# Kernel tuning notes

Hardware: AMD Instinct MI355X
Metric: run time of the kernel (lower is better)

Reference implementation:

```python
import jax, jax.numpy as jnp
import numpy as np

H, W = 256, 256
S, S_IDX, END_BIAS = 48, 3, 10
E_IDX = S - END_BIAS          # 38
N_ITER = E_IDX - (S_IDX + 1)  # 34 sequential segments after the start segment
OUT_WIN = 10                  # outlier1d window length
OUT_THRESH = 2.0


def setup_inputs() -> dict:
    key = jax.random.key(0)
    # (x, y) event coordinates in [0, W) x [0, H); t/p/b columns are unused by the module.
    events = jax.random.uniform(key, (16, 960000, 2), jnp.float32, minval=0.0, maxval=256.0)
    return {"events": events}


def _blur(a):
    """5x5 uniform (0.04) blur, SAME padding; a: [B, S, D] -> [B, S, D]."""
    k = jnp.full((1, 1, 5, 5), 0.04, jnp.float32)
    return jax.lax.conv_general_dilated(a[:, None], k, (1, 1), [(2, 2), (2, 2)])[:, 0]


def _outlier_flags(m):
    """outlier1d(m[b, si:si+10], thresh=2)[0] for si in [S_IDX+1, E_IDX). m: [B,S] -> bool [B,N_ITER]."""
    widx = (jnp.arange(N_ITER)[:, None] + S_IDX + 1) + jnp.arange(OUT_WIN)[None, :]
    w = m[:, widx]                                   # [B, N_ITER, 10]
    med = jnp.median(w, axis=-1, keepdims=True)
    diff = jnp.abs(w - med)
    mad = jnp.median(diff, axis=-1)                  # [B, N_ITER]
    return 0.6745 * diff[..., 0] / mad > OUT_THRESH


def reference(events):
    B, N, _ = events.shape
    segmentLen = N // S            # static python int
    Nu = segmentLen * S
    x = events[:, :Nu, 0].astype(jnp.int32)   # [B, Nu]
    y = events[:, :Nu, 1].astype(jnp.int32)
    chunks = jnp.repeat(jnp.arange(S), segmentLen)   # segment id per event, [Nu]
    bidx = jnp.arange(B)[:, None]

    # per-batch x-t / y-t histograms via scatter-add
    alongX = jnp.zeros((B, S, W), jnp.float32).at[bidx, chunks[None, :], x].add(1.0)
    alongY = jnp.zeros((B, S, H), jnp.float32).at[bidx, chunks[None, :], y].add(1.0)

    def proc_axis(along, D):
        flat = along.reshape(B, -1)
        cv = (flat.mean(-1) + 3.0 * jnp.std(flat, axis=-1, ddof=1))[:, None, None]
        a = _blur(jnp.clip(along, 0.0, cv))
        m = jnp.einsum('bsd,d->bs', a, jnp.arange(D, dtype=jnp.float32)) / segmentLen
        start = m[:, S_IDX:S_IDX + 1]
        aligned = jnp.round(m - start - (D // 2 - start)).astype(jnp.int32)
        return m, aligned

    meanX, alignedX = proc_axis(alongX, W)
    meanY, alignedY = proc_axis(alongY, H)
    is_out = _outlier_flags(meanX) | _outlier_flags(meanY)   # [B, N_ITER]

    def per_batch(xb, yb, aX, aY, outb):
        xs = jnp.clip(xb - aX[chunks], 0, W - 1)
        ys = jnp.clip(yb - aY[chunks], 0, H - 1)
        idx_c = (xs + W * ys).reshape(S, segmentLen)
        idx_v = (xs // 2 + (W // 2) * (ys // 2)).reshape(S, segmentLen)
        container0 = jnp.zeros(W * H, jnp.int32).at[idx_c[S_IDX]].add(1)
        ver0 = jnp.zeros((W // 2) * (H // 2), bool).at[idx_v[S_IDX]].set(True)

        def step(carry, inp):
            container, ver, stopped = carry
            ic, iv, is_o = inp
            ver_new = ver.at[iv].set(True)
            cnt = jnp.sum(ver_new).astype(jnp.float32)
            new_info = jnp.sum(jnp.logical_xor(ver_new, ver)).astype(jnp.float32)
            brk = new_info / cnt < 0.1
            do = (~stopped) & (~is_o) & (~brk)
            stopped = stopped | ((~stopped) & (~is_o) & brk)
            container = jnp.where(do, container.at[ic].add(1), container)
            ver = jnp.where(do, ver_new, ver)
            return (container, ver, stopped), None

        (container, _, _), _ = jax.lax.scan(
            step, (container0, ver0, jnp.array(False)),
            (idx_c[S_IDX + 1:E_IDX], idx_v[S_IDX + 1:E_IDX], outb))
        c = container.astype(jnp.float32)
        cv = c.mean() + 3.0 * jnp.std(c, ddof=1)
        return jnp.clip(c, 0.0, cv) / cv

    containers = jax.vmap(per_batch)(x, y, alignedX, alignedY, is_out)  # [B, W*H]
    return containers.reshape(B, 1, H, W)
```

## Files before the change

kernel.cpp:

```cpp
#include <hip/hip_runtime.h>

#define NB 16
#define NEV 960000
#define NS 48
#define SEG 20000
#define S_IDX 3
#define E_IDX 38
#define N_ITER 34
#define ND 256
#define NCH 35

__global__ __launch_bounds__(256) void hist_kernel(const float* __restrict__ events,
                                                   float* __restrict__ alongX,
                                                   float* __restrict__ alongY,
                                                   unsigned* __restrict__ compact,
                                                   unsigned* __restrict__ container,
                                                   unsigned* __restrict__ masks,
                                                   unsigned long long* __restrict__ sums,
                                                   unsigned long long* __restrict__ cvsums) {
    __shared__ unsigned hx[4][ND], hy[4][ND];
    __shared__ unsigned long long qredX[4], qredY[4];
    int tid = threadIdx.x;
    int blk = blockIdx.x;
    int b = blk / NS, c = blk % NS;
    int wave = tid >> 6, lane = tid & 63;
    #pragma unroll
    for (int j = 0; j < 4; j++) { hx[j][tid] = 0; hy[j][tid] = 0; }
    {
        uint4 z = {0u, 0u, 0u, 0u};
        for (int i = blk * 256 + tid; i < 262144; i += NB * NS * 256)
            ((uint4*)container)[i] = z;
        for (int i = blk * 256 + tid; i < 71680; i += NB * NS * 256)
            ((uint4*)masks)[i] = z;
        if (blk == 0 && tid < NB * 2) sums[tid] = 0ull;
        if (blk == 1 && tid < NB * 2) cvsums[tid] = 0ull;
    }
    __syncthreads();
    size_t base = (size_t)b * NEV + (size_t)c * SEG;
    const float4* ev4 = (const float4*)(events + base * 2);
    bool wr = (c >= S_IDX && c < E_IDX);
    uint4* dst = wr ? (uint4*)(compact + ((size_t)b * NCH + (c - S_IDX)) * (SEG / 2)) : nullptr;
    unsigned* HX = hx[wave];
    unsigned* HY = hy[wave];
    for (int k = tid; k < SEG / 8; k += 256) {
        float4 v0 = ev4[4 * k], v1 = ev4[4 * k + 1], v2 = ev4[4 * k + 2], v3 = ev4[4 * k + 3];
        int x0 = (int)v0.x, y0 = (int)v0.y, x1 = (int)v0.z, y1 = (int)v0.w;
        int x2 = (int)v1.x, y2 = (int)v1.y, x3 = (int)v1.z, y3 = (int)v1.w;
        int x4 = (int)v2.x, y4 = (int)v2.y, x5 = (int)v2.z, y5 = (int)v2.w;
        int x6 = (int)v3.x, y6 = (int)v3.y, x7 = (int)v3.z, y7 = (int)v3.w;
        x0 = x0 > 255 ? 255 : x0; y0 = y0 > 255 ? 255 : y0;
        x1 = x1 > 255 ? 255 : x1; y1 = y1 > 255 ? 255 : y1;
        x2 = x2 > 255 ? 255 : x2; y2 = y2 > 255 ? 255 : y2;
        x3 = x3 > 255 ? 255 : x3; y3 = y3 > 255 ? 255 : y3;
        x4 = x4 > 255 ? 255 : x4; y4 = y4 > 255 ? 255 : y4;
        x5 = x5 > 255 ? 255 : x5; y5 = y5 > 255 ? 255 : y5;
        x6 = x6 > 255 ? 255 : x6; y6 = y6 > 255 ? 255 : y6;
        x7 = x7 > 255 ? 255 : x7; y7 = y7 > 255 ? 255 : y7;
        atomicAdd(&HX[x0], 1u); atomicAdd(&HY[y0], 1u);
        atomicAdd(&HX[x1], 1u); atomicAdd(&HY[y1], 1u);
        atomicAdd(&HX[x2], 1u); atomicAdd(&HY[y2], 1u);
        atomicAdd(&HX[x3], 1u); atomicAdd(&HY[y3], 1u);
        atomicAdd(&HX[x4], 1u); atomicAdd(&HY[y4], 1u);
        atomicAdd(&HX[x5], 1u); atomicAdd(&HY[y5], 1u);
        atomicAdd(&HX[x6], 1u); atomicAdd(&HY[y6], 1u);
        atomicAdd(&HX[x7], 1u); atomicAdd(&HY[y7], 1u);
        if (wr) {
            uint4 p;
            p.x = (unsigned)(x0 | (y0 << 8)) | ((unsigned)(x1 | (y1 << 8)) << 16);
            p.y = (unsigned)(x2 | (y2 << 8)) | ((unsigned)(x3 | (y3 << 8)) << 16);
            p.z = (unsigned)(x4 | (y4 << 8)) | ((unsigned)(x5 | (y5 << 8)) << 16);
            p.w = (unsigned)(x6 | (y6 << 8)) | ((unsigned)(x7 | (y7 << 8)) << 16);
            dst[k] = p;
        }
    }
    __syncthreads();
    unsigned sx = hx[0][tid] + hx[1][tid] + hx[2][tid] + hx[3][tid];
    unsigned sy = hy[0][tid] + hy[1][tid] + hy[2][tid] + hy[3][tid];
    int o = (b * NS + c) * ND + tid;
    alongX[o] = (float)sx;
    alongY[o] = (float)sy;
    unsigned long long qx = (unsigned long long)sx * sx;
    unsigned long long qy = (unsigned long long)sy * sy;
    for (int off = 32; off; off >>= 1) { qx += __shfl_down(qx, off); qy += __shfl_down(qy, off); }
    if (lane == 0) { qredX[wave] = qx; qredY[wave] = qy; }
    __syncthreads();
    if (tid == 0) {
        atomicAdd(&cvsums[b * 2],     qredX[0] + qredX[1] + qredX[2] + qredX[3]);
        atomicAdd(&cvsums[b * 2 + 1], qredY[0] + qredY[1] + qredY[2] + qredY[3]);
    }
}

__global__ __launch_bounds__(256) void stats_kernel(const float* __restrict__ alongX,
                                                    const float* __restrict__ alongY,
                                                    const unsigned long long* __restrict__ cvsums,
                                                    int* __restrict__ alignedX,
                                                    int* __restrict__ alignedY,
                                                    float* __restrict__ m_all) {
    __shared__ float sbuf[16 * ND];
    int tid = threadIdx.x;
    int blk = blockIdx.x;
    int g = blk & 3, axis = (blk >> 2) & 1, b = blk >> 3;
    const float* along = (axis ? alongY : alongX) + (size_t)b * NS * ND;
    int rbase = g * 12 - 2;
    for (int j = 0; j < 16; j++) {
        int r = rbase + j;
        if (r >= 0 && r < NS) sbuf[j * ND + tid] = along[r * ND + tid];
    }
    double ts  = 960000.0;
    double ts2 = (double)cvsums[b * 2 + axis];
    const double N = (double)(NS * ND);
    double mean = ts / N;
    double var  = (ts2 - ts * ts / N) / (N - 1.0);
    float cv = (float)(mean + 3.0 * sqrt(var));
    __syncthreads();
    int wave = tid >> 6, lane = tid & 63;
    for (int q = 0; q < 3; ++q) {
        int sI = g * 12 + wave * 3 + q;
        double acc = 0.0;
        #pragma unroll
        for (int k = 0; k < 4; ++k) {
            int d = lane + 64 * k;
            int lo = d - 2 < 0 ? 0 : d - 2;
            int hi = d + 2 > 255 ? 255 : d + 2;
            double Wd = 0.5 * (double)(lo + hi) * (double)(hi - lo + 1);
            double t = 0.0;
            #pragma unroll
            for (int ds = -2; ds <= 2; ++ds) {
                int ss = sI + ds;
                if (ss >= 0 && ss < NS) t += (double)fminf(sbuf[(ss - rbase) * ND + d], cv);
            }
            acc += t * Wd;
        }
        for (int off = 32; off; off >>= 1) acc += __shfl_down(acc, off);
        if (lane == 0) {
            float mf = (float)(acc * 0.04 / (double)SEG);
            m_all[(b * 2 + axis) * NS + sI] = mf;
            (axis ? alignedY : alignedX)[b * NS + sI] = (int)rintf(mf - 128.0f);
        }
    }
}

__global__ __launch_bounds__(256) void mask_kernel(const unsigned* __restrict__ compact,
                                                   const int* __restrict__ alignedX,
                                                   const int* __restrict__ alignedY,
                                                   unsigned* __restrict__ masks) {
    __shared__ unsigned sm[512];
    int tid = threadIdx.x, blk = blockIdx.x;
    int hi = blk & 1;
    int tile = blk >> 1;
    int b = tile / NCH, ci = tile % NCH, si = S_IDX + ci;
    sm[tid] = 0; sm[tid + 256] = 0;
    __syncthreads();
    int aX = alignedX[b * NS + si], aY = alignedY[b * NS + si];
    const uint4* cp = (const uint4*)(compact + ((size_t)b * NCH + ci) * (SEG / 2));
    for (int i = hi * 1250 + tid; i < (hi + 1) * 1250; i += 256) {
        uint4 w = cp[i];
        unsigned wsv[4] = {w.x, w.y, w.z, w.w};
        #pragma unroll
        for (int j = 0; j < 4; j++) {
            unsigned v = wsv[j];
            #pragma unroll
            for (int h = 0; h < 2; h++) {
                unsigned e = (h ? (v >> 16) : v) & 0xFFFFu;
                int xs = (int)(e & 255u) - aX; xs = xs < 0 ? 0 : (xs > 255 ? 255 : xs);
                int ys = (int)(e >> 8)   - aY; ys = ys < 0 ? 0 : (ys > 255 ? 255 : ys);
                int iv = (xs >> 1) | ((ys >> 1) << 7);
                atomicOr(&sm[iv >> 5], 1u << (iv & 31));
            }
        }
    }
    __syncthreads();
    unsigned* mo = masks + (size_t)tile * 512;
    unsigned v0 = sm[tid], v1 = sm[tid + 256];
    if (v0) atomicOr(&mo[tid], v0);
    if (v1) atomicOr(&mo[tid + 256], v1);
}

__device__ inline float median10(const float* v) {
    float w[10];
    #pragma unroll
    for (int i = 0; i < 10; i++) w[i] = v[i];
    #pragma unroll
    for (int i = 1; i < 10; i++) {
        float k = w[i]; int j = i - 1;
        while (j >= 0 && w[j] > k) { w[j + 1] = w[j]; j--; }
        w[j + 1] = k;
    }
    return 0.5f * (w[4] + w[5]);
}

__device__ inline bool outlier_flag(const float* w) {
    float med = median10(w);
    float d[10];
    #pragma unroll
    for (int i = 0; i < 10; i++) d[i] = fabsf(w[i] - med);
    float d0 = d[0];
    float mad = median10(d);
    return (0.6745f * d0 / mad) > 2.0f;
}

__device__ inline unsigned wave_sum_u32(unsigned v) {
    for (int off = 32; off; off >>= 1) v += __shfl_xor(v, off);
    return v;
}

__global__ __launch_bounds__(64) void decide_kernel(const unsigned* __restrict__ masks,
                                                    const float* __restrict__ m_all,
                                                    unsigned long long* __restrict__ commitmask) {
    int b = blockIdx.x, lane = threadIdx.x;
    const unsigned* mb = masks + (size_t)b * NCH * 512;
    uint4 v0 = ((const uint4*)mb)[lane * 2];
    uint4 v1 = ((const uint4*)mb)[lane * 2 + 1];
    const uint4* pp = (const uint4*)(mb + 512);
    uint4 p0 = pp[lane * 2], p1 = pp[lane * 2 + 1];
    bool f = false;
    if (lane < N_ITER) {
        const float* mx = m_all + b * 2 * NS;
        const float* my = mx + NS;
        f = outlier_flag(&mx[S_IDX + 1 + lane]) || outlier_flag(&my[S_IDX + 1 + lane]);
    }
    unsigned long long omask = __ballot(f);
    unsigned ver[8] = {v0.x, v0.y, v0.z, v0.w, v1.x, v1.y, v1.z, v1.w};
    unsigned pc = 0;
    #pragma unroll
    for (int j = 0; j < 8; j++) pc += __popc(ver[j]);
    unsigned cnt = wave_sum_u32(pc);
    unsigned long long cm = 1ull;
    for (int idx = 1; idx < NCH; ++idx) {
        uint4 c0 = p0, c1 = p1;
        if (idx + 1 < NCH) {
            const uint4* np = (const uint4*)(mb + (size_t)(idx + 1) * 512);
            p0 = np[lane * 2]; p1 = np[lane * 2 + 1];
        }
        unsigned del[8] = {c0.x, c0.y, c0.z, c0.w, c1.x, c1.y, c1.z, c1.w};
        unsigned nl = 0;
        #pragma unroll
        for (int j = 0; j < 8; j++) nl += __popc(del[j] & ~ver[j]);
        unsigned ni = wave_sum_u32(nl);
        bool is_o = (omask >> (idx - 1)) & 1;
        if (!is_o) {
            unsigned cn = cnt + ni;
            float ratio = (float)ni / (float)cn;
            if (ratio < 0.1f) break;
            cm |= 1ull << idx;
            cnt = cn;
            #pragma unroll
            for (int j = 0; j < 8; j++) ver[j] |= del[j];
        }
    }
    if (lane == 0) commitmask[b] = cm;
}

__global__ __launch_bounds__(256) void commit_kernel(const unsigned* __restrict__ compact,
                                                     const int* __restrict__ alignedX,
                                                     const int* __restrict__ alignedY,
                                                     const unsigned long long* __restrict__ commitmask,
                                                     unsigned* __restrict__ container) {
    int blk = blockIdx.x, tid = threadIdx.x;
    int qi = blk & 3;
    int tile = blk >> 2;
    int b = tile / NCH, ci = tile % NCH;
    if (!((commitmask[b] >> ci) & 1ull)) return;
    int si = S_IDX + ci;
    int aX = alignedX[b * NS + si], aY = alignedY[b * NS + si];
    unsigned* cont = container + (size_t)b * 65536;
    const uint4* cp = (const uint4*)(compact + ((size_t)b * NCH + ci) * (SEG / 2));
    for (int i = qi * 625 + tid; i < (qi + 1) * 625; i += 256) {
        uint4 w = cp[i];
        unsigned wsv[4] = {w.x, w.y, w.z, w.w};
        #pragma unroll
        for (int j = 0; j < 4; j++) {
            unsigned v = wsv[j];
            #pragma unroll
            for (int h = 0; h < 2; h++) {
                unsigned e = (h ? (v >> 16) : v) & 0xFFFFu;
                int xs = (int)(e & 255u) - aX; xs = xs < 0 ? 0 : (xs > 255 ? 255 : xs);
                int ys = (int)(e >> 8)   - aY; ys = ys < 0 ? 0 : (ys > 255 ? 255 : ys);
                atomicAdd(&cont[xs | (ys << 8)], 1u);
            }
        }
    }
}

__global__ __launch_bounds__(256) void cv_kernel(const unsigned* __restrict__ container,
                                                 unsigned long long* __restrict__ sums) {
    __shared__ unsigned long long sredA[4], sredB[4];
    int tid = threadIdx.x, blk = blockIdx.x;
    int b = blk >> 4, part = blk & 15;
    const uint4* c4 = (const uint4*)(container + (size_t)b * 65536) + part * 1024;
    unsigned long long s = 0, s2 = 0;
    for (int i = tid; i < 1024; i += 256) {
        uint4 v = c4[i];
        s  += (unsigned long long)v.x + v.y + v.z + v.w;
        s2 += (unsigned long long)v.x * v.x + (unsigned long long)v.y * v.y
            + (unsigned long long)v.z * v.z + (unsigned long long)v.w * v.w;
    }
    for (int off = 32; off; off >>= 1) { s += __shfl_down(s, off); s2 += __shfl_down(s2, off); }
    if ((tid & 63) == 0) { sredA[tid >> 6] = s; sredB[tid >> 6] = s2; }
    __syncthreads();
    if (tid == 0) {
        atomicAdd(&sums[b * 2],     sredA[0] + sredA[1] + sredA[2] + sredA[3]);
        atomicAdd(&sums[b * 2 + 1], sredB[0] + sredB[1] + sredB[2] + sredB[3]);
    }
}

__global__ __launch_bounds__(256) void finish_kernel(const unsigned* __restrict__ container,
                                                     const unsigned long long* __restrict__ sums,
                                                     float* __restrict__ out) {
    int g = blockIdx.x * 256 + threadIdx.x;
    int b = g >> 14;
    double ts  = (double)sums[b * 2];
    double ts2 = (double)sums[b * 2 + 1];
    double mean = ts / 65536.0;
    double var  = (ts2 - ts * ts / 65536.0) / 65535.0;
    float cv = (float)(mean + 3.0 * sqrt(var));
    uint4 v = ((const uint4*)container)[g];
    float4 o;
    o.x = fminf((float)v.x, cv) / cv;
    o.y = fminf((float)v.y, cv) / cv;
    o.z = fminf((float)v.z, cv) / cv;
    o.w = fminf((float)v.w, cv) / cv;
    ((float4*)out)[g] = o;
}

extern "C" void kernel_launch(void* const* d_in, const int* in_sizes, int n_in,
                              void* d_out, int out_size, void* d_ws, size_t ws_size,
                              hipStream_t stream) {
    const float* events = (const float*)d_in[0];
    float* out = (float*)d_out;
    char* ws = (char*)d_ws;

    float*    alongX    = (float*)(ws);
    float*    alongY    = (float*)(ws + 786432);
    unsigned* container = (unsigned*)(ws + 1572864);
    int*      alignedX  = (int*)(ws + 5767168);
    int*      alignedY  = (int*)(ws + 5770240);
    float*    m_all     = (float*)(ws + 5773312);
    unsigned long long* commitmask = (unsigned long long*)(ws + 5779456);
    unsigned long long* sums       = (unsigned long long*)(ws + 5779584);
    unsigned long long* cvsums     = (unsigned long long*)(ws + 5779840);
    unsigned* compact   = (unsigned*)(ws + 6291456);
    unsigned* masks     = (unsigned*)(ws + 29360128);

    hist_kernel<<<NB * NS, 256, 0, stream>>>(events, alongX, alongY, compact,
                                             container, masks, sums, cvsums);
    stats_kernel<<<NB * 2 * 4, 256, 0, stream>>>(alongX, alongY, cvsums,
                                                 alignedX, alignedY, m_all);
    mask_kernel<<<NB * NCH * 2, 256, 0, stream>>>(compact, alignedX, alignedY, masks);
    decide_kernel<<<NB, 64, 0, stream>>>(masks, m_all, commitmask);
    commit_kernel<<<NB * NCH * 4, 256, 0, stream>>>(compact, alignedX, alignedY,
                                                    commitmask, container);
    cv_kernel<<<NB * 16, 256, 0, stream>>>(container, sums);
    finish_kernel<<<1024, 256, 0, stream>>>(container, sums, out);
}
```

Before: 269.4 us.

## Fold stats into mask/decide kernels and merge cv with finish

Drops the separate stats kernel. The mask kernel now recomputes the two centroids it needs directly from the histograms, and the decide kernel recomputes all centroids per batch, writing the aligned offsets and keeping m in LDS. The cv reduction and the normalize pass are merged into a single per-batch kernel of 1024 threads, which removes the atomics and the sums buffer. This cuts the pipeline from seven launches to five, at the cost of redundant centroid work and only 16 blocks for both the decide and final kernels.

```diff
diff --git a/kernel.cpp b/kernel.cpp
--- a/kernel.cpp
+++ b/kernel.cpp
@@ -10,13 +10,46 @@
 #define ND 256
 #define NCH 35
 
+__device__ inline void centroid(const float* __restrict__ along,
+                                float cv, int sI, int lane,
+                                float* mf_out, int* ai_out) {
+    double acc = 0.0;
+    #pragma unroll
+    for (int k = 0; k < 4; ++k) {
+        int d = lane + 64 * k;
+        int lo = d - 2 < 0 ? 0 : d - 2;
+        int hi = d + 2 > 255 ? 255 : d + 2;
+        double Wd = 0.5 * (double)(lo + hi) * (double)(hi - lo + 1);
+        double t = 0.0;
+        #pragma unroll
+        for (int ds = -2; ds <= 2; ++ds) {
+            int ss = sI + ds;
+            if (ss >= 0 && ss < NS) t += (double)fminf(along[ss * ND + d], cv);
+        }
+        acc += t * Wd;
+    }
+    for (int off = 32; off; off >>= 1) acc += __shfl_down(acc, off);
+    float mf = (float)(acc * 0.04 / (double)SEG);
+    *mf_out = mf;
+    *ai_out = (int)rintf(mf - 128.0f);
+}
+
+__device__ inline float cv_from_sums(const unsigned long long* __restrict__ cvsums,
+                                     int b, int axis) {
+    double ts  = 960000.0;
+    double ts2 = (double)cvsums[b * 2 + axis];
+    const double N = (double)(NS * ND);
+    double mean = ts / N;
+    double var  = (ts2 - ts * ts / N) / (N - 1.0);
+    return (float)(mean + 3.0 * sqrt(var));
+}
+
 __global__ __launch_bounds__(256) void hist_kernel(const float* __restrict__ events,
                                                    float* __restrict__ alongX,
                                                    float* __restrict__ alongY,
                                                    unsigned* __restrict__ compact,
                                                    unsigned* __restrict__ container,
                                                    unsigned* __restrict__ masks,
-                                                   unsigned long long* __restrict__ sums,
                                                    unsigned long long* __restrict__ cvsums) {
     __shared__ unsigned hx[4][ND], hy[4][ND];
     __shared__ unsigned long long qredX[4], qredY[4];
@@ -32,8 +65,7 @@
             ((uint4*)container)[i] = z;
         for (int i = blk * 256 + tid; i < 71680; i += NB * NS * 256)
             ((uint4*)masks)[i] = z;
-        if (blk == 0 && tid < NB * 2) sums[tid] = 0ull;
-        if (blk == 1 && tid < NB * 2) cvsums[tid] = 0ull;
+        if (blk == 0 && tid < NB * 2) cvsums[tid] = 0ull;
     }
     __syncthreads();
     size_t base = (size_t)b * NEV + (size_t)c * SEG;
@@ -90,68 +122,28 @@
     }
 }
 
-__global__ __launch_bounds__(256) void stats_kernel(const float* __restrict__ alongX,
-                                                    const float* __restrict__ alongY,
-                                                    const unsigned long long* __restrict__ cvsums,
-                                                    int* __restrict__ alignedX,
-                                                    int* __restrict__ alignedY,
-                                                    float* __restrict__ m_all) {
-    __shared__ float sbuf[16 * ND];
-    int tid = threadIdx.x;
-    int blk = blockIdx.x;
-    int g = blk & 3, axis = (blk >> 2) & 1, b = blk >> 3;
-    const float* along = (axis ? alongY : alongX) + (size_t)b * NS * ND;
-    int rbase = g * 12 - 2;
-    for (int j = 0; j < 16; j++) {
-        int r = rbase + j;
-        if (r >= 0 && r < NS) sbuf[j * ND + tid] = along[r * ND + tid];
-    }
-    double ts  = 960000.0;
-    double ts2 = (double)cvsums[b * 2 + axis];
-    const double N = (double)(NS * ND);
-    double mean = ts / N;
-    double var  = (ts2 - ts * ts / N) / (N - 1.0);
-    float cv = (float)(mean + 3.0 * sqrt(var));
-    __syncthreads();
-    int wave = tid >> 6, lane = tid & 63;
-    for (int q = 0; q < 3; ++q) {
-        int sI = g * 12 + wave * 3 + q;
-        double acc = 0.0;
-        #pragma unroll
-        for (int k = 0; k < 4; ++k) {
-            int d = lane + 64 * k;
-            int lo = d - 2 < 0 ? 0 : d - 2;
-            int hi = d + 2 > 255 ? 255 : d + 2;
-            double Wd = 0.5 * (double)(lo + hi) * (double)(hi - lo + 1);
-            double t = 0.0;
-            #pragma unroll
-            for (int ds = -2; ds <= 2; ++ds) {
-                int ss = sI + ds;
-                if (ss >= 0 && ss < NS) t += (double)fminf(sbuf[(ss - rbase) * ND + d], cv);
-            }
-            acc += t * Wd;
-        }
-        for (int off = 32; off; off >>= 1) acc += __shfl_down(acc, off);
-        if (lane == 0) {
-            float mf = (float)(acc * 0.04 / (double)SEG);
-            m_all[(b * 2 + axis) * NS + sI] = mf;
-            (axis ? alignedY : alignedX)[b * NS + sI] = (int)rintf(mf - 128.0f);
-        }
-    }
-}
-
 __global__ __launch_bounds__(256) void mask_kernel(const unsigned* __restrict__ compact,
-                                                   const int* __restrict__ alignedX,
-                                                   const int* __restrict__ alignedY,
+                                                   const float* __restrict__ alongX,
+                                                   const float* __restrict__ alongY,
+                                                   const unsigned long long* __restrict__ cvsums,
                                                    unsigned* __restrict__ masks) {
     __shared__ unsigned sm[512];
+    __shared__ int sal[2];
     int tid = threadIdx.x, blk = blockIdx.x;
     int hi = blk & 1;
     int tile = blk >> 1;
     int b = tile / NCH, ci = tile % NCH, si = S_IDX + ci;
+    int wave = tid >> 6, lane = tid & 63;
     sm[tid] = 0; sm[tid + 256] = 0;
-    __syncthreads();
-    int aX = alignedX[b * NS + si], aY = alignedY[b * NS + si];
+    if (wave < 2) {
+        const float* along = (wave ? alongY : alongX) + (size_t)b * NS * ND;
+        float cv = cv_from_sums(cvsums, b, wave);
+        float mf; int ai;
+        centroid(along, cv, si, lane, &mf, &ai);
+        if (lane == 0) sal[wave] = ai;
+    }
+    __syncthreads();
+    int aX = sal[0], aY = sal[1];
     const uint4* cp = (const uint4*)(compact + ((size_t)b * NCH + ci) * (SEG / 2));
     for (int i = hi * 1250 + tid; i < (hi + 1) * 1250; i += 256) {
         uint4 w = cp[i];
@@ -204,51 +196,74 @@
     return v;
 }
 
-__global__ __launch_bounds__(64) void decide_kernel(const unsigned* __restrict__ masks,
-                                                    const float* __restrict__ m_all,
-                                                    unsigned long long* __restrict__ commitmask) {
-    int b = blockIdx.x, lane = threadIdx.x;
-    const unsigned* mb = masks + (size_t)b * NCH * 512;
-    uint4 v0 = ((const uint4*)mb)[lane * 2];
-    uint4 v1 = ((const uint4*)mb)[lane * 2 + 1];
-    const uint4* pp = (const uint4*)(mb + 512);
-    uint4 p0 = pp[lane * 2], p1 = pp[lane * 2 + 1];
-    bool f = false;
-    if (lane < N_ITER) {
-        const float* mx = m_all + b * 2 * NS;
-        const float* my = mx + NS;
-        f = outlier_flag(&mx[S_IDX + 1 + lane]) || outlier_flag(&my[S_IDX + 1 + lane]);
-    }
-    unsigned long long omask = __ballot(f);
-    unsigned ver[8] = {v0.x, v0.y, v0.z, v0.w, v1.x, v1.y, v1.z, v1.w};
-    unsigned pc = 0;
-    #pragma unroll
-    for (int j = 0; j < 8; j++) pc += __popc(ver[j]);
-    unsigned cnt = wave_sum_u32(pc);
-    unsigned long long cm = 1ull;
-    for (int idx = 1; idx < NCH; ++idx) {
-        uint4 c0 = p0, c1 = p1;
-        if (idx + 1 < NCH) {
-            const uint4* np = (const uint4*)(mb + (size_t)(idx + 1) * 512);
-            p0 = np[lane * 2]; p1 = np[lane * 2 + 1];
-        }
-        unsigned del[8] = {c0.x, c0.y, c0.z, c0.w, c1.x, c1.y, c1.z, c1.w};
-        unsigned nl = 0;
-        #pragma unroll
-        for (int j = 0; j < 8; j++) nl += __popc(del[j] & ~ver[j]);
-        unsigned ni = wave_sum_u32(nl);
-        bool is_o = (omask >> (idx - 1)) & 1;
-        if (!is_o) {
-            unsigned cn = cnt + ni;
-            float ratio = (float)ni / (float)cn;
-            if (ratio < 0.1f) break;
-            cm |= 1ull << idx;
-            cnt = cn;
+__global__ __launch_bounds__(256) void decide_kernel(const unsigned* __restrict__ masks,
+                                                     const float* __restrict__ alongX,
+                                                     const float* __restrict__ alongY,
+                                                     const unsigned long long* __restrict__ cvsums,
+                                                     int* __restrict__ alignedX,
+                                                     int* __restrict__ alignedY,
+                                                     unsigned long long* __restrict__ commitmask) {
+    __shared__ float mlds[2 * NS];
+    int b = blockIdx.x, tid = threadIdx.x;
+    int wave = tid >> 6, lane = tid & 63;
+    float cv0 = cv_from_sums(cvsums, b, 0);
+    float cv1 = cv_from_sums(cvsums, b, 1);
+    for (int q = 0; q < 24; ++q) {
+        int p = wave + 4 * q;
+        int ax = p >= NS;
+        int sI = p - NS * ax;
+        const float* along = (ax ? alongY : alongX) + (size_t)b * NS * ND;
+        float mf; int ai;
+        centroid(along, ax ? cv1 : cv0, sI, lane, &mf, &ai);
+        if (lane == 0) {
+            mlds[ax * NS + sI] = mf;
+            (ax ? alignedY : alignedX)[b * NS + sI] = ai;
+        }
+    }
+    __syncthreads();
+    if (tid < 64) {
+        const unsigned* mb = masks + (size_t)b * NCH * 512;
+        uint4 v0 = ((const uint4*)mb)[lane * 2];
+        uint4 v1 = ((const uint4*)mb)[lane * 2 + 1];
+        const uint4* pp = (const uint4*)(mb + 512);
+        uint4 p0 = pp[lane * 2], p1 = pp[lane * 2 + 1];
+        bool f = false;
+        if (lane < N_ITER) {
+            const float* mx = &mlds[0];
+            const float* my = &mlds[NS];
+            f = outlier_flag(&mx[S_IDX + 1 + lane]) || outlier_flag(&my[S_IDX + 1 + lane]);
+        }
+        unsigned long long omask = __ballot(f);
+        unsigned ver[8] = {v0.x, v0.y, v0.z, v0.w, v1.x, v1.y, v1.z, v1.w};
+        unsigned pc = 0;
+        #pragma unroll
+        for (int j = 0; j < 8; j++) pc += __popc(ver[j]);
+        unsigned cnt = wave_sum_u32(pc);
+        unsigned long long cm = 1ull;
+        for (int idx = 1; idx < NCH; ++idx) {
+            uint4 c0 = p0, c1 = p1;
+            if (idx + 1 < NCH) {
+                const uint4* np = (const uint4*)(mb + (size_t)(idx + 1) * 512);
+                p0 = np[lane * 2]; p1 = np[lane * 2 + 1];
+            }
+            unsigned del[8] = {c0.x, c0.y, c0.z, c0.w, c1.x, c1.y, c1.z, c1.w};
+            unsigned nl = 0;
             #pragma unroll
-            for (int j = 0; j < 8; j++) ver[j] |= del[j];
-        }
-    }
-    if (lane == 0) commitmask[b] = cm;
+            for (int j = 0; j < 8; j++) nl += __popc(del[j] & ~ver[j]);
+            unsigned ni = wave_sum_u32(nl);
+            bool is_o = (omask >> (idx - 1)) & 1;
+            if (!is_o) {
+                unsigned cn = cnt + ni;
+                float ratio = (float)ni / (float)cn;
+                if (ratio < 0.1f) break;
+                cm |= 1ull << idx;
+                cnt = cn;
+                #pragma unroll
+                for (int j = 0; j < 8; j++) ver[j] |= del[j];
+            }
+        }
+        if (lane == 0) commitmask[b] = cm;
+    }
 }
 
 __global__ __launch_bounds__(256) void commit_kernel(const unsigned* __restrict__ compact,
@@ -282,45 +297,44 @@
     }
 }
 
-__global__ __launch_bounds__(256) void cv_kernel(const unsigned* __restrict__ container,
-                                                 unsigned long long* __restrict__ sums) {
-    __shared__ unsigned long long sredA[4], sredB[4];
-    int tid = threadIdx.x, blk = blockIdx.x;
-    int b = blk >> 4, part = blk & 15;
-    const uint4* c4 = (const uint4*)(container + (size_t)b * 65536) + part * 1024;
+__global__ __launch_bounds__(1024) void cvfinish_kernel(const unsigned* __restrict__ container,
+                                                        float* __restrict__ out) {
+    __shared__ unsigned long long sA[16], sB[16];
+    __shared__ float cvs;
+    int b = blockIdx.x, tid = threadIdx.x;
+    const uint4* c4 = (const uint4*)(container + (size_t)b * 65536);
     unsigned long long s = 0, s2 = 0;
-    for (int i = tid; i < 1024; i += 256) {
+    for (int i = tid; i < 16384; i += 1024) {
         uint4 v = c4[i];
         s  += (unsigned long long)v.x + v.y + v.z + v.w;
         s2 += (unsigned long long)v.x * v.x + (unsigned long long)v.y * v.y
             + (unsigned long long)v.z * v.z + (unsigned long long)v.w * v.w;
     }
     for (int off = 32; off; off >>= 1) { s += __shfl_down(s, off); s2 += __shfl_down(s2, off); }
-    if ((tid & 63) == 0) { sredA[tid >> 6] = s; sredB[tid >> 6] = s2; }
+    if ((tid & 63) == 0) { sA[tid >> 6] = s; sB[tid >> 6] = s2; }
     __syncthreads();
     if (tid == 0) {
-        atomicAdd(&sums[b * 2],     sredA[0] + sredA[1] + sredA[2] + sredA[3]);
-        atomicAdd(&sums[b * 2 + 1], sredB[0] + sredB[1] + sredB[2] + sredB[3]);
-    }
-}
-
-__global__ __launch_bounds__(256) void finish_kernel(const unsigned* __restrict__ container,
-                                                     const unsigned long long* __restrict__ sums,
-                                                     float* __restrict__ out) {
-    int g = blockIdx.x * 256 + threadIdx.x;
-    int b = g >> 14;
-    double ts  = (double)sums[b * 2];
-    double ts2 = (double)sums[b * 2 + 1];
-    double mean = ts / 65536.0;
-    double var  = (ts2 - ts * ts / 65536.0) / 65535.0;
-    float cv = (float)(mean + 3.0 * sqrt(var));
-    uint4 v = ((const uint4*)container)[g];
-    float4 o;
-    o.x = fminf((float)v.x, cv) / cv;
-    o.y = fminf((float)v.y, cv) / cv;
-    o.z = fminf((float)v.z, cv) / cv;
-    o.w = fminf((float)v.w, cv) / cv;
-    ((float4*)out)[g] = o;
+        unsigned long long S = 0, S2 = 0;
+        #pragma unroll
+        for (int w = 0; w < 16; w++) { S += sA[w]; S2 += sB[w]; }
+        double ts  = (double)S;
+        double ts2 = (double)S2;
+        double mean = ts / 65536.0;
+        double var  = (ts2 - ts * ts / 65536.0) / 65535.0;
+        cvs = (float)(mean + 3.0 * sqrt(var));
+    }
+    __syncthreads();
+    float cv = cvs;
+    float4* o4 = (float4*)out + (size_t)b * 16384;
+    for (int i = tid; i < 16384; i += 1024) {
+        uint4 v = c4[i];
+        float4 o;
+        o.x = fminf((float)v.x, cv) / cv;
+        o.y = fminf((float)v.y, cv) / cv;
+        o.z = fminf((float)v.z, cv) / cv;
+        o.w = fminf((float)v.w, cv) / cv;
+        o4[i] = o;
+    }
 }
 
 extern "C" void kernel_launch(void* const* d_in, const int* in_sizes, int n_in,
@@ -335,21 +349,17 @@
     unsigned* container = (unsigned*)(ws + 1572864);
     int*      alignedX  = (int*)(ws + 5767168);
     int*      alignedY  = (int*)(ws + 5770240);
-    float*    m_all     = (float*)(ws + 5773312);
     unsigned long long* commitmask = (unsigned long long*)(ws + 5779456);
-    unsigned long long* sums       = (unsigned long long*)(ws + 5779584);
     unsigned long long* cvsums     = (unsigned long long*)(ws + 5779840);
     unsigned* compact   = (unsigned*)(ws + 6291456);
     unsigned* masks     = (unsigned*)(ws + 29360128);
 
     hist_kernel<<<NB * NS, 256, 0, stream>>>(events, alongX, alongY, compact,
-                                             container, masks, sums, cvsums);
-    stats_kernel<<<NB * 2 * 4, 256, 0, stream>>>(alongX, alongY, cvsums,
-                                                 alignedX, alignedY, m_all);
-    mask_kernel<<<NB * NCH * 2, 256, 0, stream>>>(compact, alignedX, alignedY, masks);
-    decide_kernel<<<NB, 64, 0, stream>>>(masks, m_all, commitmask);
+                                             container, masks, cvsums);
+    mask_kernel<<<NB * NCH * 2, 256, 0, stream>>>(compact, alongX, alongY, cvsums, masks);
+    decide_kernel<<<NB, 256, 0, stream>>>(masks, alongX, alongY, cvsums,
+                                          alignedX, alignedY, commitmask);
     commit_kernel<<<NB * NCH * 4, 256, 0, stream>>>(compact, alignedX, alignedY,
                                                     commitmask, container);
-    cv_kernel<<<NB * 16, 256, 0, stream>>>(container, sums);
-    finish_kernel<<<1024, 256, 0, stream>>>(container, sums, out);
-}
+    cvfinish_kernel<<<NB, 1024, 0, stream>>>(container, out);
+}
```

Result: slower. 346.4 us (+28.6%).
